# Optimization experiments

Measured on AMD Instinct MI355X. Metric: run time of the kernel, lower is better.

## Reference

```python
import jax, jax.numpy as jnp
import numpy as np

B, SEQ, D, N_LAYERS, HEADS, D_FF = 256, 43, 18, 6, 3, 2048
A_MAX, NB = 128, 7
EPS = 1e-6


def _norm(x, a, b):
    mu = x.mean(-1, keepdims=True)
    sd = jnp.std(x, axis=-1, ddof=1, keepdims=True)  # torch std is unbiased
    return a * (x - mu) / (sd + EPS) + b


def _attn(x, Wq, bq, Wk, bk, Wv, bv, Wo, bo, mask):
    b_, s, d = x.shape
    dk = d // HEADS
    def split_heads(W, bb):
        return (x @ W + bb).reshape(b_, s, HEADS, dk).transpose(0, 2, 1, 3)
    q, k, v = split_heads(Wq, bq), split_heads(Wk, bk), split_heads(Wv, bv)
    scores = jnp.einsum('bhqd,bhkd->bhqk', q, k) / jnp.sqrt(jnp.float32(dk))
    scores = jnp.where(mask[:, None, :, :] == 0, -1e9, scores)  # mask [B,1,S] -> [B,1,1,S]
    attn = jax.nn.softmax(scores, axis=-1)
    o = jnp.einsum('bhqk,bhkd->bhqd', attn, v).transpose(0, 2, 1, 3).reshape(b_, s, d)
    return o @ Wo + bo


def setup_inputs() -> dict:
    key = jax.random.key(0)
    ks = iter(jax.random.split(key, 40))
    g = lambda shape, s=0.05: jax.random.normal(next(ks), shape, dtype=jnp.float32) * s
    inp = {
        'src': jax.random.normal(next(ks), (B, SEQ, D), dtype=jnp.float32),
        'mask': jnp.ones((B, 1, SEQ), dtype=jnp.int32),
        'max_atoms': A_MAX,
        'enc_Wq': g((N_LAYERS, D, D)), 'enc_bq': g((N_LAYERS, D)),
        'enc_Wk': g((N_LAYERS, D, D)), 'enc_bk': g((N_LAYERS, D)),
        'enc_Wv': g((N_LAYERS, D, D)), 'enc_bv': g((N_LAYERS, D)),
        'enc_Wo': g((N_LAYERS, D, D)), 'enc_bo': g((N_LAYERS, D)),
        'enc_ln1_a': jnp.ones((N_LAYERS, D), jnp.float32), 'enc_ln1_b': jnp.zeros((N_LAYERS, D), jnp.float32),
        'enc_ln2_a': jnp.ones((N_LAYERS, D), jnp.float32), 'enc_ln2_b': jnp.zeros((N_LAYERS, D), jnp.float32),
        'enc_ffW1': g((N_LAYERS, D, D_FF)), 'enc_ffb1': g((N_LAYERS, D_FF)),
        'enc_ffW2': g((N_LAYERS, D_FF, D)), 'enc_ffb2': g((N_LAYERS, D)),
        'll2_W': g((D, A_MAX)), 'll2_b': g((A_MAX,)),
        'll_W': g((SEQ, A_MAX)), 'll_b': g((A_MAX,)),
        'fl_W': g((2 * A_MAX, NB)), 'fl_b': g((NB,)),
    }
    return inp


def reference(src, enc_Wq, enc_bq, enc_Wk, enc_bk, enc_Wv, enc_bv, enc_Wo, enc_bo,
              enc_ln1_a, enc_ln1_b, enc_ln2_a, enc_ln2_b,
              enc_ffW1, enc_ffb1, enc_ffW2, enc_ffb2,
              ll2_W, ll2_b, ll_W, ll_b, fl_W, fl_b, mask, max_atoms):
    # --- Encoder (dropout=0 at eval; no final norm, as in source) ---
    x = src
    for i in range(N_LAYERS):
        x2 = _norm(x, enc_ln1_a[i], enc_ln1_b[i])
        x = x + _attn(x2, enc_Wq[i], enc_bq[i], enc_Wk[i], enc_bk[i],
                      enc_Wv[i], enc_bv[i], enc_Wo[i], enc_bo[i], mask)
        x2 = _norm(x, enc_ln2_a[i], enc_ln2_b[i])
        x = x + (jax.nn.relu(x2 @ enc_ffW1[i] + enc_ffb1[i]) @ enc_ffW2[i] + enc_ffb2[i])
    # --- EdgeClassify2 ---
    red = x @ ll2_W + ll2_b            # [B, S, A]
    red = red.transpose(0, 2, 1)       # [B, A, S]
    R = red @ ll_W + ll_b              # [B, A, A]; repeat_e[:,i,i,:] == R[:,i,:]
    # final_e[b,i,j] = concat(R[b,i], R[b,j]); fl(concat) = R_i@W1 + R_j@W2 + b (exact)
    W1, W2 = fl_W[:max_atoms], fl_W[max_atoms:]
    P = R @ W1                          # [B, A, nb]
    Q = R @ W2                          # [B, A, nb]
    return P[:, :, None, :] + Q[:, None, :, :] + fl_b  # [B, A, A, nb]
```

## Files before the change

### kernel.cpp

```cpp
#include <hip/hip_runtime.h>
#include <math.h>

namespace {

constexpr int Sq = 43;
constexpr int Dm = 18;
constexpr int Dff = 2048;
constexpr int Am = 128;
constexpr int Nb = 7;
constexpr int NR = 11008;
constexpr int RSZ = NR * Dm;
constexpr int WROW = 20;
constexpr float EPSf = 1e-6f;

typedef float v2f __attribute__((ext_vector_type(2)));
typedef float v4f __attribute__((ext_vector_type(4)));

__global__ __launch_bounds__(64) void k_attn(
    int layer,
    const float* __restrict__ Xi, float* __restrict__ Xn,
    float* __restrict__ x2g,
    const int* __restrict__ maskg,
    const float* __restrict__ Wq, const float* __restrict__ bq,
    const float* __restrict__ Wk, const float* __restrict__ bk,
    const float* __restrict__ Wv, const float* __restrict__ bv,
    const float* __restrict__ ln1a, const float* __restrict__ ln1b,
    const float* __restrict__ Wo, const float* __restrict__ bo,
    const float* __restrict__ ln2a, const float* __restrict__ ln2b,
    const float* __restrict__ b2g,
    const float* __restrict__ fW1g, const float* __restrict__ fb1g,
    const float* __restrict__ fW2g,
    float* __restrict__ W1P, float* __restrict__ W2P,
    const float* __restrict__ llW, const float* __restrict__ llb,
    const float* __restrict__ flW, const float* __restrict__ flb,
    const float* __restrict__ ll2b,
    float* __restrict__ Mw, float* __restrict__ PS1, float* __restrict__ QS2)
{
    __shared__ __align__(16) float ks[Sq * 20];
    __shared__ __align__(16) float vs[Sq * 20];
    __shared__ int ms[Sq];
    __shared__ float M[602];
    __shared__ float cc2[14];
    __shared__ float SS[14];

    const int tid = threadIdx.x;
    const int b = blockIdx.x;

    if (b >= 256) {
        if (b < 448) {
            const int idx = (b - 256) * 64 + tid;
            const int l = idx / Dff;
            const int j = idx - l * Dff;
            float* o1 = W1P + (size_t)idx * WROW;
            float* o2 = W2P + (size_t)idx * WROW;
            #pragma unroll
            for (int d = 0; d < Dm; d++)
                o1[d] = fW1g[(size_t)l * Dm * Dff + (size_t)d * Dff + j];
            o1[18] = fb1g[l * Dff + j];
            o1[19] = 0.f;
            #pragma unroll
            for (int d = 0; d < Dm; d++)
                o2[d] = fW2g[((size_t)l * Dff + j) * Dm + d];
            o2[18] = 0.f;
            o2[19] = 0.f;
            if (idx < WROW) {
                W1P[(size_t)6 * Dff * WROW + idx] = 0.f;
                W2P[(size_t)6 * Dff * WROW + idx] = 0.f;
            }
            return;
        }
        for (int m = tid; m < 602; m += 64) {
            int half = m / 301, rem = m - half * 301;
            int s = rem / 7, n = rem - 7 * s;
            float a = 0.f;
            for (int jj = 0; jj < Am; jj++)
                a += llW[s * Am + jj] * flW[(half * Am + jj) * Nb + n];
            M[m] = a;
        }
        if (tid < 14) {
            int half = tid / 7, n = tid - 7 * (tid / 7);
            float a = 0.f;
            for (int jj = 0; jj < Am; jj++)
                a += llb[jj] * flW[(half * Am + jj) * Nb + n];
            cc2[tid] = a;
        }
        __syncthreads();
        if (tid < 14) {
            int half = tid / 7, n = tid - 7 * (tid / 7);
            float s2 = 0.f;
            for (int s = 0; s < Sq; s++) s2 += M[half * 301 + s * 7 + n];
            SS[tid] = s2;
        }
        __syncthreads();
        for (int m = tid; m < 602; m += 64) Mw[m] = M[m];
        for (int m = tid; m < 896; m += 64) {
            int i = m / 7, n = m - 7 * i;
            PS1[m] = cc2[n] + ll2b[i] * SS[n];
            QS2[m] = cc2[7 + n] + ll2b[i] * SS[7 + n] + flb[n];
        }
        return;
    }

    const float scale = 0.40824829046386296f;

    if (tid < Sq) ms[tid] = maskg[b * Sq + tid];

    float y[Dm];
    float qv[Dm];
    if (tid < Sq) {
        const size_t ro = (size_t)(b * Sq + tid) * Dm;
        #pragma unroll
        for (int k = 0; k < 9; k++) {
            float2 t = *(const float2*)(Xi + ro + 2 * k);
            y[2 * k] = t.x; y[2 * k + 1] = t.y;
        }
        float mu = 0.f;
        #pragma unroll
        for (int d = 0; d < Dm; d++) mu += y[d];
        mu *= (1.f / Dm);
        float var = 0.f;
        #pragma unroll
        for (int d = 0; d < Dm; d++) { float t = y[d] - mu; var += t * t; }
        var *= (1.f / (Dm - 1));
        float isd = 1.f / (sqrtf(var) + EPSf);
        float x2[Dm];
        #pragma unroll
        for (int d = 0; d < Dm; d++)
            x2[d] = ln1a[layer * Dm + d] * (y[d] - mu) * isd
                  + ln1b[layer * Dm + d];
        const float* wqp = Wq + layer * Dm * Dm;
        const float* wkp = Wk + layer * Dm * Dm;
        const float* wvp = Wv + layer * Dm * Dm;
        #pragma unroll 3
        for (int d = 0; d < Dm; d++) {
            float aq = bq[layer * Dm + d];
            float ak = bk[layer * Dm + d];
            float av = bv[layer * Dm + d];
            #pragma unroll
            for (int dd = 0; dd < Dm; dd++) {
                aq += x2[dd] * wqp[dd * Dm + d];
                ak += x2[dd] * wkp[dd * Dm + d];
                av += x2[dd] * wvp[dd * Dm + d];
            }
            qv[d] = aq;
            ks[tid * 20 + d] = ak;
            vs[tid * 20 + d] = av;
        }
    }
    __syncthreads();
    if (tid >= Sq) return;

    float o[Dm];
    #pragma unroll
    for (int h = 0; h < 3; h++) {
        float sum = 0.f;
        float o6[6];
        #pragma unroll
        for (int d = 0; d < 6; d++) o6[d] = 0.f;
        const float q0 = qv[h * 6], q1 = qv[h * 6 + 1], q2 = qv[h * 6 + 2];
        const float q3 = qv[h * 6 + 3], q4 = qv[h * 6 + 4], q5 = qv[h * 6 + 5];
        for (int j = 0; j < Sq; j++) {
            const float* kr = ks + j * 20 + h * 6;
            const float2 k0 = *(const float2*)(kr);
            const float2 k1 = *(const float2*)(kr + 2);
            const float2 k2 = *(const float2*)(kr + 4);
            float t = q0 * k0.x + q1 * k0.y + q2 * k1.x +
                      q3 * k1.y + q4 * k2.x + q5 * k2.y;
            t *= scale;
            if (ms[j] == 0) t = -1e9f;
            float e = __expf(t);
            sum += e;
            const float* vr = vs + j * 20 + h * 6;
            const float2 v0 = *(const float2*)(vr);
            const float2 v1 = *(const float2*)(vr + 2);
            const float2 v2 = *(const float2*)(vr + 4);
            o6[0] += e * v0.x; o6[1] += e * v0.y; o6[2] += e * v1.x;
            o6[3] += e * v1.y; o6[4] += e * v2.x; o6[5] += e * v2.y;
        }
        float inv = 1.f / sum;
        #pragma unroll
        for (int d = 0; d < 6; d++) o[h * 6 + d] = o6[d] * inv;
    }

    const float* wo = Wo + layer * Dm * Dm;
    float yo[Dm];
    #pragma unroll 3
    for (int d = 0; d < Dm; d++) {
        float t = bo[layer * Dm + d];
        #pragma unroll
        for (int dd = 0; dd < Dm; dd++) t += o[dd] * wo[dd * Dm + d];
        yo[d] = y[d] + t;
    }
    const size_t ro = (size_t)(b * Sq + tid) * Dm;
    #pragma unroll
    for (int d = 0; d < Dm; d++)
        Xn[ro + d] = yo[d] + b2g[layer * Dm + d];
    float mu = 0.f;
    #pragma unroll
    for (int d = 0; d < Dm; d++) mu += yo[d];
    mu *= (1.f / Dm);
    float var = 0.f;
    #pragma unroll
    for (int d = 0; d < Dm; d++) { float t = yo[d] - mu; var += t * t; }
    var *= (1.f / (Dm - 1));
    float isd = 1.f / (sqrtf(var) + EPSf);
    #pragma unroll
    for (int d = 0; d < Dm; d++)
        x2g[ro + d] =
            ln2a[layer * Dm + d] * (yo[d] - mu) * isd + ln2b[layer * Dm + d];
}

__global__ __launch_bounds__(256, 3) void k_ffn(
    int layer, const float* __restrict__ x2g,
    const float* __restrict__ W1P, const float* __restrict__ W2P,
    float* __restrict__ Xn)
{
    __shared__ float Ls[4 * 128 * Dm];

    const int tid  = threadIdx.x;
    const int lane = tid & 63;
    const int wv   = __builtin_amdgcn_readfirstlane(tid >> 6);
    const int rg   = blockIdx.x >> 3;
    const int q    = blockIdx.x & 7;
    const int row0 = rg * 128 + lane;
    const int row1 = row0 + 64;
    const int j0   = q * 256 + wv * 64;

    const v4f* w1p = (const v4f*)(W1P + ((size_t)layer * Dff + j0) * WROW);
    const v4f* w2p = (const v4f*)(W2P + ((size_t)layer * Dff + j0) * WROW);

    v2f xp0[9], xp1[9];
    #pragma unroll
    for (int k = 0; k < 9; k++) {
        xp0[k] = *(const v2f*)(x2g + (size_t)row0 * Dm + 2 * k);
        xp1[k] = *(const v2f*)(x2g + (size_t)row1 * Dm + 2 * k);
    }

    v2f acc0[9], acc1[9];
    #pragma unroll
    for (int k = 0; k < 9; k++) {
        acc0[k] = (v2f){0.f, 0.f};
        acc1[k] = (v2f){0.f, 0.f};
    }

    #pragma unroll 2
    for (int jj = 0; jj < 64; jj++) {
        const v4f a0 = w1p[jj * 5 + 0], a1 = w1p[jj * 5 + 1],
                  a2 = w1p[jj * 5 + 2], a3 = w1p[jj * 5 + 3],
                  a4 = w1p[jj * 5 + 4];
        const v4f c0 = w2p[jj * 5 + 0], c1 = w2p[jj * 5 + 1],
                  c2 = w2p[jj * 5 + 2], c3 = w2p[jj * 5 + 3],
                  c4 = w2p[jj * 5 + 4];

        v2f h2a = xp0[0] * a0.lo;
        h2a = __builtin_elementwise_fma(xp0[1], a0.hi, h2a);
        h2a = __builtin_elementwise_fma(xp0[2], a1.lo, h2a);
        h2a = __builtin_elementwise_fma(xp0[3], a1.hi, h2a);
        h2a = __builtin_elementwise_fma(xp0[4], a2.lo, h2a);
        h2a = __builtin_elementwise_fma(xp0[5], a2.hi, h2a);
        h2a = __builtin_elementwise_fma(xp0[6], a3.lo, h2a);
        h2a = __builtin_elementwise_fma(xp0[7], a3.hi, h2a);
        h2a = __builtin_elementwise_fma(xp0[8], a4.lo, h2a);
        float ha = a4.z + h2a.x + h2a.y;
        ha = fmaxf(ha, 0.f);
        const v2f hha = {ha, ha};

        v2f h2b = xp1[0] * a0.lo;
        h2b = __builtin_elementwise_fma(xp1[1], a0.hi, h2b);
        h2b = __builtin_elementwise_fma(xp1[2], a1.lo, h2b);
        h2b = __builtin_elementwise_fma(xp1[3], a1.hi, h2b);
        h2b = __builtin_elementwise_fma(xp1[4], a2.lo, h2b);
        h2b = __builtin_elementwise_fma(xp1[5], a2.hi, h2b);
        h2b = __builtin_elementwise_fma(xp1[6], a3.lo, h2b);
        h2b = __builtin_elementwise_fma(xp1[7], a3.hi, h2b);
        h2b = __builtin_elementwise_fma(xp1[8], a4.lo, h2b);
        float hb = a4.z + h2b.x + h2b.y;
        hb = fmaxf(hb, 0.f);
        const v2f hhb = {hb, hb};

        acc0[0] = __builtin_elementwise_fma(hha, c0.lo, acc0[0]);
        acc0[1] = __builtin_elementwise_fma(hha, c0.hi, acc0[1]);
        acc0[2] = __builtin_elementwise_fma(hha, c1.lo, acc0[2]);
        acc0[3] = __builtin_elementwise_fma(hha, c1.hi, acc0[3]);
        acc0[4] = __builtin_elementwise_fma(hha, c2.lo, acc0[4]);
        acc0[5] = __builtin_elementwise_fma(hha, c2.hi, acc0[5]);
        acc0[6] = __builtin_elementwise_fma(hha, c3.lo, acc0[6]);
        acc0[7] = __builtin_elementwise_fma(hha, c3.hi, acc0[7]);
        acc0[8] = __builtin_elementwise_fma(hha, c4.lo, acc0[8]);

        acc1[0] = __builtin_elementwise_fma(hhb, c0.lo, acc1[0]);
        acc1[1] = __builtin_elementwise_fma(hhb, c0.hi, acc1[1]);
        acc1[2] = __builtin_elementwise_fma(hhb, c1.lo, acc1[2]);
        acc1[3] = __builtin_elementwise_fma(hhb, c1.hi, acc1[3]);
        acc1[4] = __builtin_elementwise_fma(hhb, c2.lo, acc1[4]);
        acc1[5] = __builtin_elementwise_fma(hhb, c2.hi, acc1[5]);
        acc1[6] = __builtin_elementwise_fma(hhb, c3.lo, acc1[6]);
        acc1[7] = __builtin_elementwise_fma(hhb, c3.hi, acc1[7]);
        acc1[8] = __builtin_elementwise_fma(hhb, c4.lo, acc1[8]);
    }

    #pragma unroll
    for (int k = 0; k < 9; k++) {
        Ls[(wv * 128 + lane) * Dm + 2 * k]       = acc0[k].x;
        Ls[(wv * 128 + lane) * Dm + 2 * k + 1]   = acc0[k].y;
        Ls[(wv * 128 + lane + 64) * Dm + 2 * k]     = acc1[k].x;
        Ls[(wv * 128 + lane + 64) * Dm + 2 * k + 1] = acc1[k].y;
    }
    __syncthreads();
    for (int e = tid; e < 2304; e += 256) {
        float s = Ls[e] + Ls[2304 + e] + Ls[4608 + e] + Ls[6912 + e];
        unsafeAtomicAdd(&Xn[(size_t)rg * 2304 + e], s);
    }
}

__global__ __launch_bounds__(256) void k_out(
    const float* __restrict__ xg,
    const float* __restrict__ ll2W,
    const float* __restrict__ Mw, const float* __restrict__ PS1,
    const float* __restrict__ QS2, float* __restrict__ out)
{
    __shared__ float xb[Sq * Dm];
    __shared__ float M[602];
    __shared__ float T[2][Dm][Nb];
    __shared__ float Pc[32 * Nb];
    __shared__ float QBs[Am * Nb];

    const int b = blockIdx.y, chunk = blockIdx.x, tid = threadIdx.x;

    for (int e = tid; e < Sq * Dm; e += 256)
        xb[e] = xg[(size_t)b * (Sq * Dm) + e];
    for (int m = tid; m < 602; m += 256) M[m] = Mw[m];
    __syncthreads();

    for (int m = tid; m < 252; m += 256) {
        int half = m / 126, rem = m - half * 126;
        int d = rem / 7, n = rem - 7 * d;
        float a = 0.f;
        for (int s = 0; s < Sq; s++)
            a += xb[s * Dm + d] * M[half * 301 + s * 7 + n];
        T[half][d][n] = a;
    }
    __syncthreads();

    for (int m = tid; m < 224; m += 256) {
        int il = m / 7, n = m - 7 * il;
        int i = chunk * 32 + il;
        float a = PS1[i * 7 + n];
        #pragma unroll
        for (int d = 0; d < Dm; d++) a += T[0][d][n] * ll2W[d * Am + i];
        Pc[m] = a;
    }
    for (int e = tid; e < 896; e += 256) {
        int jj = e / 7, n = e - 7 * jj;
        float a = QS2[e];
        #pragma unroll
        for (int d = 0; d < Dm; d++) a += T[1][d][n] * ll2W[d * Am + jj];
        QBs[e] = a;
    }
    __syncthreads();

    if (tid < 224) {
        const int e = 4 * tid;
        const float q0 = QBs[e], q1 = QBs[e + 1], q2 = QBs[e + 2], q3 = QBs[e + 3];
        const int n0 = e % 7, n1 = (e + 1) % 7, n2 = (e + 2) % 7, n3 = (e + 3) % 7;
        const size_t base = (size_t)b * (Am * Am * Nb)
                          + (size_t)chunk * 32 * 896 + e;
        for (int il = 0; il < 32; il++) {
            const float* pc = Pc + il * 7;
            float4 v;
            v.x = pc[n0] + q0; v.y = pc[n1] + q1;
            v.z = pc[n2] + q2; v.w = pc[n3] + q3;
            *(float4*)(out + base + (size_t)il * 896) = v;
        }
    }
}

}

extern "C" void kernel_launch(void* const* d_in, const int* in_sizes, int n_in,
                              void* d_out, int out_size, void* d_ws, size_t ws_size,
                              hipStream_t stream)
{
    (void)in_sizes; (void)n_in; (void)out_size; (void)ws_size;

    const float* src  = (const float*)d_in[0];
    const int*   mask = (const int*)  d_in[1];
    const float* Wq   = (const float*)d_in[3];
    const float* bq   = (const float*)d_in[4];
    const float* Wk   = (const float*)d_in[5];
    const float* bk   = (const float*)d_in[6];
    const float* Wv   = (const float*)d_in[7];
    const float* bv   = (const float*)d_in[8];
    const float* Wo   = (const float*)d_in[9];
    const float* bo   = (const float*)d_in[10];
    const float* ln1a = (const float*)d_in[11];
    const float* ln1b = (const float*)d_in[12];
    const float* ln2a = (const float*)d_in[13];
    const float* ln2b = (const float*)d_in[14];
    const float* fW1  = (const float*)d_in[15];
    const float* fb1  = (const float*)d_in[16];
    const float* fW2  = (const float*)d_in[17];
    const float* fb2  = (const float*)d_in[18];
    const float* ll2W = (const float*)d_in[19];
    const float* ll2b = (const float*)d_in[20];
    const float* llW  = (const float*)d_in[21];
    const float* llb  = (const float*)d_in[22];
    const float* flW  = (const float*)d_in[23];
    const float* flb  = (const float*)d_in[24];
    float* out = (float*)d_out;

    const size_t WPSZ = (size_t)6 * Dff * WROW + WROW;

    float* ws  = (float*)d_ws;
    float* xA  = ws;
    float* xB  = ws + 1 * (size_t)RSZ;
    float* x2g = ws + 2 * (size_t)RSZ;
    float* W1P = ws + 3 * (size_t)RSZ;
    float* W2P = W1P + WPSZ;
    float* Mw  = W2P + WPSZ;
    float* PS1 = Mw + 604;
    float* QS2 = PS1 + 896;

    for (int i = 0; i < 6; i++) {
        const float* Xi = (i == 0) ? src : ((i % 2 == 1) ? xB : xA);
        float*       Xn = (i % 2 == 0) ? xB : xA;
        const int nblk = (i == 0) ? 449 : 256;
        k_attn<<<nblk, 64, 0, stream>>>(i, Xi, Xn, x2g, mask,
                                        Wq, bq, Wk, bk, Wv, bv,
                                        ln1a, ln1b, Wo, bo, ln2a, ln2b, fb2,
                                        fW1, fb1, fW2, W1P, W2P,
                                        llW, llb, flW, flb, ll2b,
                                        Mw, PS1, QS2);
        k_ffn<<<688, 256, 0, stream>>>(i, x2g, W1P, W2P, Xn);
    }
    k_out<<<dim3(4, 256), 256, 0, stream>>>(xA, ll2W, Mw, PS1, QS2, out);
}
```

Before: 524.1 us.

## Split attention heads across waves and software-prefetch FFN weights

The attention kernel now launches 192 threads per block, one wave per head. Each wave computes that head's Q/K/V slice and softmax. The per-head outputs are staged in shared memory, and wave 0 then does the output projection and the second layernorm. This spreads the serial per-token work across three waves. Separately, the FFN inner loop loads the next iteration's weight vectors ahead of use to hide load latency. That prefetch reads one row past the 64-row tile, which appears to rely on the padded tail, and it raises register pressure.

Result: faster. 495.4 us (-5.5%).

```diff
diff --git a/kernel.cpp b/kernel.cpp
--- a/kernel.cpp
+++ b/kernel.cpp
@@ -16,7 +16,7 @@
 typedef float v2f __attribute__((ext_vector_type(2)));
 typedef float v4f __attribute__((ext_vector_type(4)));
 
-__global__ __launch_bounds__(64) void k_attn(
+__global__ __launch_bounds__(192) void k_attn(
     int layer,
     const float* __restrict__ Xi, float* __restrict__ Xn,
     float* __restrict__ x2g,
@@ -38,6 +38,7 @@
 {
     __shared__ __align__(16) float ks[Sq * 20];
     __shared__ __align__(16) float vs[Sq * 20];
+    __shared__ float os[Sq * Dm];
     __shared__ int ms[Sq];
     __shared__ float M[602];
     __shared__ float cc2[14];
@@ -47,8 +48,8 @@
     const int b = blockIdx.x;
 
     if (b >= 256) {
-        if (b < 448) {
-            const int idx = (b - 256) * 64 + tid;
+        if (b < 320) {
+            const int idx = (b - 256) * 192 + tid;
             const int l = idx / Dff;
             const int j = idx - l * Dff;
             float* o1 = W1P + (size_t)idx * WROW;
@@ -69,7 +70,7 @@
             }
             return;
         }
-        for (int m = tid; m < 602; m += 64) {
+        for (int m = tid; m < 602; m += 192) {
             int half = m / 301, rem = m - half * 301;
             int s = rem / 7, n = rem - 7 * s;
             float a = 0.f;
@@ -92,8 +93,8 @@
             SS[tid] = s2;
         }
         __syncthreads();
-        for (int m = tid; m < 602; m += 64) Mw[m] = M[m];
-        for (int m = tid; m < 896; m += 64) {
+        for (int m = tid; m < 602; m += 192) Mw[m] = M[m];
+        for (int m = tid; m < 896; m += 192) {
             int i = m / 7, n = m - 7 * i;
             PS1[m] = cc2[n] + ll2b[i] * SS[n];
             QS2[m] = cc2[7 + n] + ll2b[i] * SS[7 + n] + flb[n];
@@ -102,13 +103,15 @@
     }
 
     const float scale = 0.40824829046386296f;
+    const int h = tid >> 6;
+    const int q = tid & 63;
 
     if (tid < Sq) ms[tid] = maskg[b * Sq + tid];
 
     float y[Dm];
-    float qv[Dm];
-    if (tid < Sq) {
-        const size_t ro = (size_t)(b * Sq + tid) * Dm;
+    float qv6[6];
+    if (q < Sq) {
+        const size_t ro = (size_t)(b * Sq + q) * Dm;
         #pragma unroll
         for (int k = 0; k < 9; k++) {
             float2 t = *(const float2*)(Xi + ro + 2 * k);
@@ -131,8 +134,9 @@
         const float* wqp = Wq + layer * Dm * Dm;
         const float* wkp = Wk + layer * Dm * Dm;
         const float* wvp = Wv + layer * Dm * Dm;
-        #pragma unroll 3
-        for (int d = 0; d < Dm; d++) {
+        #pragma unroll
+        for (int dh = 0; dh < 6; dh++) {
+            const int d = h * 6 + dh;
             float aq = bq[layer * Dm + d];
             float ak = bk[layer * Dm + d];
             float av = bv[layer * Dm + d];
@@ -142,23 +146,20 @@
                 ak += x2[dd] * wkp[dd * Dm + d];
                 av += x2[dd] * wvp[dd * Dm + d];
             }
-            qv[d] = aq;
-            ks[tid * 20 + d] = ak;
-            vs[tid * 20 + d] = av;
-        }
-    }
-    __syncthreads();
-    if (tid >= Sq) return;
-
-    float o[Dm];
-    #pragma unroll
-    for (int h = 0; h < 3; h++) {
+            qv6[dh] = aq;
+            ks[q * 20 + d] = ak;
+            vs[q * 20 + d] = av;
+        }
+    }
+    __syncthreads();
+
+    if (q < Sq) {
         float sum = 0.f;
         float o6[6];
         #pragma unroll
         for (int d = 0; d < 6; d++) o6[d] = 0.f;
-        const float q0 = qv[h * 6], q1 = qv[h * 6 + 1], q2 = qv[h * 6 + 2];
-        const float q3 = qv[h * 6 + 3], q4 = qv[h * 6 + 4], q5 = qv[h * 6 + 5];
+        const float q0 = qv6[0], q1 = qv6[1], q2 = qv6[2];
+        const float q3 = qv6[3], q4 = qv6[4], q5 = qv6[5];
         for (int j = 0; j < Sq; j++) {
             const float* kr = ks + j * 20 + h * 6;
             const float2 k0 = *(const float2*)(kr);
@@ -179,35 +180,39 @@
         }
         float inv = 1.f / sum;
         #pragma unroll
-        for (int d = 0; d < 6; d++) o[h * 6 + d] = o6[d] * inv;
-    }
-
-    const float* wo = Wo + layer * Dm * Dm;
-    float yo[Dm];
-    #pragma unroll 3
-    for (int d = 0; d < Dm; d++) {
-        float t = bo[layer * Dm + d];
-        #pragma unroll
-        for (int dd = 0; dd < Dm; dd++) t += o[dd] * wo[dd * Dm + d];
-        yo[d] = y[d] + t;
-    }
-    const size_t ro = (size_t)(b * Sq + tid) * Dm;
-    #pragma unroll
-    for (int d = 0; d < Dm; d++)
-        Xn[ro + d] = yo[d] + b2g[layer * Dm + d];
-    float mu = 0.f;
-    #pragma unroll
-    for (int d = 0; d < Dm; d++) mu += yo[d];
-    mu *= (1.f / Dm);
-    float var = 0.f;
-    #pragma unroll
-    for (int d = 0; d < Dm; d++) { float t = yo[d] - mu; var += t * t; }
-    var *= (1.f / (Dm - 1));
-    float isd = 1.f / (sqrtf(var) + EPSf);
-    #pragma unroll
-    for (int d = 0; d < Dm; d++)
-        x2g[ro + d] =
-            ln2a[layer * Dm + d] * (yo[d] - mu) * isd + ln2b[layer * Dm + d];
+        for (int d = 0; d < 6; d++) os[q * Dm + h * 6 + d] = o6[d] * inv;
+    }
+    __syncthreads();
+
+    if (h == 0 && q < Sq) {
+        const float* wo = Wo + layer * Dm * Dm;
+        const float* orow = os + q * Dm;
+        float yo[Dm];
+        #pragma unroll 3
+        for (int d = 0; d < Dm; d++) {
+            float t = bo[layer * Dm + d];
+            #pragma unroll
+            for (int dd = 0; dd < Dm; dd++) t += orow[dd] * wo[dd * Dm + d];
+            yo[d] = y[d] + t;
+        }
+        const size_t ro = (size_t)(b * Sq + q) * Dm;
+        #pragma unroll
+        for (int d = 0; d < Dm; d++)
+            Xn[ro + d] = yo[d] + b2g[layer * Dm + d];
+        float mu = 0.f;
+        #pragma unroll
+        for (int d = 0; d < Dm; d++) mu += yo[d];
+        mu *= (1.f / Dm);
+        float var = 0.f;
+        #pragma unroll
+        for (int d = 0; d < Dm; d++) { float t = yo[d] - mu; var += t * t; }
+        var *= (1.f / (Dm - 1));
+        float isd = 1.f / (sqrtf(var) + EPSf);
+        #pragma unroll
+        for (int d = 0; d < Dm; d++)
+            x2g[ro + d] =
+                ln2a[layer * Dm + d] * (yo[d] - mu) * isd + ln2b[layer * Dm + d];
+    }
 }
 
 __global__ __launch_bounds__(256, 3) void k_ffn(
@@ -243,14 +248,14 @@
         acc1[k] = (v2f){0.f, 0.f};
     }
 
-    #pragma unroll 2
+    v4f a0 = w1p[0], a1 = w1p[1], a2 = w1p[2], a3 = w1p[3], a4 = w1p[4];
+    v4f c0 = w2p[0], c1 = w2p[1], c2 = w2p[2], c3 = w2p[3], c4 = w2p[4];
+
     for (int jj = 0; jj < 64; jj++) {
-        const v4f a0 = w1p[jj * 5 + 0], a1 = w1p[jj * 5 + 1],
-                  a2 = w1p[jj * 5 + 2], a3 = w1p[jj * 5 + 3],
-                  a4 = w1p[jj * 5 + 4];
-        const v4f c0 = w2p[jj * 5 + 0], c1 = w2p[jj * 5 + 1],
-                  c2 = w2p[jj * 5 + 2], c3 = w2p[jj * 5 + 3],
-                  c4 = w2p[jj * 5 + 4];
+        const v4f* n1 = w1p + (jj + 1) * 5;
+        const v4f* n2 = w2p + (jj + 1) * 5;
+        const v4f na0 = n1[0], na1 = n1[1], na2 = n1[2], na3 = n1[3], na4 = n1[4];
+        const v4f nc0 = n2[0], nc1 = n2[1], nc2 = n2[2], nc3 = n2[3], nc4 = n2[4];
 
         v2f h2a = xp0[0] * a0.lo;
         h2a = __builtin_elementwise_fma(xp0[1], a0.hi, h2a);
@@ -297,12 +302,15 @@
         acc1[6] = __builtin_elementwise_fma(hhb, c3.lo, acc1[6]);
         acc1[7] = __builtin_elementwise_fma(hhb, c3.hi, acc1[7]);
         acc1[8] = __builtin_elementwise_fma(hhb, c4.lo, acc1[8]);
+
+        a0 = na0; a1 = na1; a2 = na2; a3 = na3; a4 = na4;
+        c0 = nc0; c1 = nc1; c2 = nc2; c3 = nc3; c4 = nc4;
     }
 
     #pragma unroll
     for (int k = 0; k < 9; k++) {
-        Ls[(wv * 128 + lane) * Dm + 2 * k]       = acc0[k].x;
-        Ls[(wv * 128 + lane) * Dm + 2 * k + 1]   = acc0[k].y;
+        Ls[(wv * 128 + lane) * Dm + 2 * k]          = acc0[k].x;
+        Ls[(wv * 128 + lane) * Dm + 2 * k + 1]      = acc0[k].y;
         Ls[(wv * 128 + lane + 64) * Dm + 2 * k]     = acc1[k].x;
         Ls[(wv * 128 + lane + 64) * Dm + 2 * k + 1] = acc1[k].y;
     }
@@ -424,13 +432,13 @@
     for (int i = 0; i < 6; i++) {
         const float* Xi = (i == 0) ? src : ((i % 2 == 1) ? xB : xA);
         float*       Xn = (i % 2 == 0) ? xB : xA;
-        const int nblk = (i == 0) ? 449 : 256;
-        k_attn<<<nblk, 64, 0, stream>>>(i, Xi, Xn, x2g, mask,
-                                        Wq, bq, Wk, bk, Wv, bv,
-                                        ln1a, ln1b, Wo, bo, ln2a, ln2b, fb2,
-                                        fW1, fb1, fW2, W1P, W2P,
-                                        llW, llb, flW, flb, ll2b,
-                                        Mw, PS1, QS2);
+        const int nblk = (i == 0) ? 321 : 256;
+        k_attn<<<nblk, 192, 0, stream>>>(i, Xi, Xn, x2g, mask,
+                                         Wq, bq, Wk, bk, Wv, bv,
+                                         ln1a, ln1b, Wo, bo, ln2a, ln2b, fb2,
+                                         fW1, fb1, fW2, W1P, W2P,
+                                         llW, llb, flW, flb, ll2b,
+                                         Mw, PS1, QS2);
         k_ffn<<<688, 256, 0, stream>>>(i, x2g, W1P, W2P, Xn);
     }
     k_out<<<dim3(4, 256), 256, 0, stream>>>(xA, ll2W, Mw, PS1, QS2, out);
```
